# Kernel tuning notes

Measured on AMD Instinct MI355X. Metric: run time of the kernel, lower is better.

Reference implementation:

```python
import jax, jax.numpy as jnp
import numpy as np

EMB = 512
HEADS = 16
WH, WW = 8, 8
N = WH * WW
B = 2048
CPB_HID = 512
EPS = 1e-12


def _buffers():
    # continuous relative coords table, shape (1, 2*WH-1, 2*WW-1, 2)
    ch = np.arange(-(WH - 1), WH, dtype=np.float32)
    cw = np.arange(-(WW - 1), WW, dtype=np.float32)
    t = np.stack(np.meshgrid(ch, cw, indexing='ij')).transpose(1, 2, 0)[None].copy()
    t[..., 0] /= (WH - 1)
    t[..., 1] /= (WW - 1)
    t *= 8.0
    t = np.sign(t) * np.log2(np.abs(t) + 1.0) / np.log2(8.0)
    # relative position index, shape (N, N), values in [0, (2*WH-1)*(2*WW-1))
    coords = np.stack(np.meshgrid(np.arange(WH), np.arange(WW), indexing='ij'))
    cf = coords.reshape(2, -1)
    rel = (cf[:, :, None] - cf[:, None, :]).transpose(1, 2, 0).copy()
    rel[..., 0] += WH - 1
    rel[..., 1] += WW - 1
    rel[..., 0] *= 2 * WW - 1
    idx = rel.sum(-1)
    return jnp.asarray(t, jnp.float32), jnp.asarray(idx, jnp.int32)


def setup_inputs() -> dict:
    key = jax.random.key(0)
    ks = jax.random.split(key, 8)
    rel_table, rel_index = _buffers()
    s = 0.02
    return {
        'x': jax.random.normal(ks[0], (B, N, EMB), jnp.float32),
        'qkv_w': jax.random.normal(ks[1], (3 * EMB, EMB), jnp.float32) * s,
        'q_bias': jnp.zeros((EMB,), jnp.float32),
        'v_bias': jnp.zeros((EMB,), jnp.float32),
        'flex_attn': jnp.full((HEADS, 1, 1), np.log(10.0), jnp.float32),
        'cpb_w1': jax.random.normal(ks[2], (CPB_HID, 2), jnp.float32) * s,
        'cpb_b1': jnp.zeros((CPB_HID,), jnp.float32),
        'cpb_w2': jax.random.normal(ks[3], (HEADS, CPB_HID), jnp.float32) * s,
        'proj_w': jax.random.normal(ks[4], (EMB, EMB), jnp.float32) * s,
        'proj_b': jnp.zeros((EMB,), jnp.float32),
        'rel_table': rel_table,
        'rel_index': rel_index,
    }


def reference(x, qkv_w, q_bias, v_bias, flex_attn, cpb_w1, cpb_b1, cpb_w2,
              proj_w, proj_b, rel_table, rel_index):
    Bx, Nx, C = x.shape
    H = HEADS
    D = C // H
    # qkv with bias only on q and v (k bias is zero), as in the torch code
    qkv_bias = jnp.concatenate([q_bias, jnp.zeros_like(v_bias), v_bias])
    qkv = x @ qkv_w.T + qkv_bias                      # (B, N, 3C)
    qkv = qkv.reshape(Bx, Nx, 3, H, D).transpose(2, 0, 3, 1, 4)
    q, k, v = qkv[0], qkv[1], qkv[2]                  # each (B, H, N, D)
    # cosine attention: L2-normalize q and k
    qn = q / jnp.maximum(jnp.linalg.norm(q, axis=-1, keepdims=True), EPS)
    kn = k / jnp.maximum(jnp.linalg.norm(k, axis=-1, keepdims=True), EPS)
    attn = jnp.einsum('bhnd,bhmd->bhnm', qn, kn)      # (B, H, N, N)
    # learned per-head temperature, clamped at 1/0.01
    scale = jnp.exp(jnp.minimum(flex_attn, jnp.log(jnp.float32(100.0))))  # (H,1,1)
    attn = attn * scale[None]
    # continuous relative position bias via MLP + gather
    bias_tab = jax.nn.relu(rel_table @ cpb_w1.T + cpb_b1) @ cpb_w2.T      # (1, 2WH-1, 2WW-1, H)
    bias_tab = bias_tab.reshape(-1, H)
    bias = bias_tab[rel_index.reshape(-1)].reshape(Nx, Nx, H)
    bias = 16.0 * jax.nn.sigmoid(bias.transpose(2, 0, 1))                 # (H, N, N)
    attn = jax.nn.softmax(attn + bias[None], axis=-1)
    out = jnp.einsum('bhnm,bhmd->bhnd', attn, v)      # (B, H, N, D)
    out = out.transpose(0, 2, 1, 3).reshape(Bx, Nx, C)
    return out @ proj_w.T + proj_b
```

## Files before the change

### kernel.cpp

```cpp
#include <hip/hip_runtime.h>

using bf16x8 = __attribute__((ext_vector_type(8))) short;
using f32x4  = __attribute__((ext_vector_type(4))) float;
using f32x16 = __attribute__((ext_vector_type(16))) float;

static constexpr int EMB = 512, HEADS = 16, NTOK = 64, BWIN = 2048;
static constexpr int MROWS = BWIN * NTOK;
static constexpr int QKVN  = 3 * EMB;

__device__ __forceinline__ float bf2f(unsigned int u) {
  union { unsigned int i; float f; } c; c.i = u << 16; return c.f;
}
__device__ __forceinline__ unsigned short f2bf(float x) {
  union { float f; unsigned int i; } c; c.f = x;
  return (unsigned short)((c.i + 0x7fffu + ((c.i >> 16) & 1u)) >> 16);
}
__device__ __forceinline__ void gload_lds16(const void* g, void* l) {
  __builtin_amdgcn_global_load_lds((const __attribute__((address_space(1))) void*)g,
                                   (__attribute__((address_space(3))) void*)l, 16, 0, 0);
}
__device__ __forceinline__ unsigned int cvt_pk_bf16(float lo, float hi) {
  unsigned int d;
  asm("v_cvt_pk_bf16_f32 %0, %1, %2" : "=v"(d) : "v"(lo), "v"(hi));
  return d;
}

#define BARRIER() __builtin_amdgcn_s_barrier()
#define LGKM0()  do { asm volatile("s_waitcnt lgkmcnt(0)" ::: "memory"); \
                      __builtin_amdgcn_sched_barrier(0); } while (0)
#define VMCNT2() do { asm volatile("s_waitcnt vmcnt(2)" ::: "memory"); \
                      __builtin_amdgcn_sched_barrier(0); } while (0)

__global__ __launch_bounds__(256) void xcast(const float* __restrict__ x,
                                             unsigned short* __restrict__ xb) {
  size_t i = ((size_t)blockIdx.x * 256 + threadIdx.x) * 8;
  float4 a = *(const float4*)(x + i);
  float4 b = *(const float4*)(x + i + 4);
  ushort4 lo = make_ushort4(f2bf(a.x), f2bf(a.y), f2bf(a.z), f2bf(a.w));
  ushort4 hi = make_ushort4(f2bf(b.x), f2bf(b.y), f2bf(b.z), f2bf(b.w));
  *(ushort4*)(xb + i) = lo;
  *(ushort4*)(xb + i + 4) = hi;
}

__global__ void prep_weights(const float* __restrict__ qkv_w, const float* __restrict__ proj_w,
                             const float* __restrict__ q_bias, const float* __restrict__ v_bias,
                             unsigned short* __restrict__ wq, unsigned short* __restrict__ wp,
                             float* __restrict__ qkv_bias) {
  int i = blockIdx.x * 256 + threadIdx.x;
  wq[i] = f2bf(qkv_w[i]);
  if (i < EMB * EMB) wp[i] = f2bf(proj_w[i]);
  if (i < EMB) {
    qkv_bias[i]           = q_bias[i];
    qkv_bias[EMB + i]     = 0.f;
    qkv_bias[2 * EMB + i] = v_bias[i];
  }
}

__global__ __launch_bounds__(64) void cpb_mlp(const float* __restrict__ tbl,
                        const float* __restrict__ w1, const float* __restrict__ b1,
                        const float* __restrict__ w2, float* __restrict__ tab) {
  __shared__ float hid[512];
  const int p = blockIdx.x, t = threadIdx.x;
  const float t0 = tbl[p * 2], t1 = tbl[p * 2 + 1];
  #pragma unroll
  for (int s = 0; s < 8; ++s) {
    int j = t + s * 64;
    hid[j] = fmaxf(0.f, t0 * w1[j * 2] + t1 * w1[j * 2 + 1] + b1[j]);
  }
  __syncthreads();
  const int h = t >> 2, q = t & 3;
  float sum = 0.f;
  for (int j = q * 128; j < q * 128 + 128; ++j) sum += hid[j] * w2[h * 512 + j];
  sum += __shfl_xor(sum, 1);
  sum += __shfl_xor(sum, 2);
  if (q == 0) tab[p * 16 + h] = sum;
}

__global__ void cpb_expand(const float* __restrict__ tab, const int* __restrict__ rel_index,
                           float* __restrict__ biasT) {
  int e = blockIdx.x * 256 + threadIdx.x;
  int h = e >> 12, ij = e & 4095;
  int kk = ij >> 6, q = ij & 63;
  float x = tab[rel_index[q * 64 + kk] * 16 + h];
  biasT[e] = 16.f / (1.f + __expf(-x));
}

template<bool OUT_F32, int NBX, int KT>
__global__ __launch_bounds__(512, 2) void gemm256(const unsigned short* __restrict__ Ap,
    const unsigned short* __restrict__ Bp, const float* __restrict__ bias,
    void* __restrict__ Cp, int M, int N) {
  __shared__ unsigned short As[2][256 * 64];
  __shared__ unsigned short Bs[2][256 * 64];
  constexpr int NT = KT / 64;
  constexpr int NITER = NT / 2;
  const int t = threadIdx.x;
  const int l = t & 63, w = t >> 6;
  const int lr = l & 15, lg = l >> 4;
  const int q8 = gridDim.x >> 3;
  const int wgid = (blockIdx.x & 7) * q8 + (blockIdx.x >> 3);
  const int n0 = (wgid % NBX) * 256, m0 = (wgid / NBX) * 256;
  const int wm = (w >> 2) * 128, wn = (w & 3) * 64;
  const int ha128 = (w >> 2) * 128;
  const int srow = t >> 3;
  const int scol = ((t & 7) ^ (srow & 7)) << 3;
  const unsigned short* Abase = Ap + (size_t)m0 * KT;
  const unsigned short* Bbase = Bp + (size_t)n0 * KT;

  f32x4 acc[8][4];
  #pragma unroll
  for (int i = 0; i < 8; ++i)
    #pragma unroll
    for (int j = 0; j < 4; ++j) acc[i][j] = (f32x4){0.f, 0.f, 0.f, 0.f};
  bf16x8 afr[4][2], bfr[4][2];

  auto stage_half = [&](int d, int kt, int half, bool isA) {
    const unsigned short* g = (isA ? Abase : Bbase)
        + (size_t)(half * 128 + srow) * KT + kt * 64 + scol;
    unsigned short* lds = (isA ? &As[d][0] : &Bs[d][0]) + half * 8192 + (t >> 6) * 512;
    gload_lds16(g, lds);
    gload_lds16(g + (size_t)64 * KT, lds + 4096);
  };
  auto ldA4 = [&](int d, int mb) {
    #pragma unroll
    for (int m = 0; m < 4; ++m) {
      int row = ha128 + (mb + m) * 16 + lr;
      #pragma unroll
      for (int ks = 0; ks < 2; ++ks)
        afr[m][ks] = *(const bf16x8*)(&As[d][row * 64 + ((((ks << 2) + lg) ^ (lr & 7)) << 3)]);
    }
  };
  auto ldB2 = [&](int d, int nb) {
    #pragma unroll
    for (int n = 0; n < 2; ++n) {
      int row = wn + (nb + n) * 16 + lr;
      #pragma unroll
      for (int ks = 0; ks < 2; ++ks)
        bfr[nb + n][ks] = *(const bf16x8*)(&Bs[d][row * 64 + ((((ks << 2) + lg) ^ (lr & 7)) << 3)]);
    }
  };
  auto mfmaQ = [&](int mb, int nb) {
    __builtin_amdgcn_s_setprio(1);
    #pragma unroll
    for (int ks = 0; ks < 2; ++ks)
      #pragma unroll
      for (int m = 0; m < 4; ++m)
        #pragma unroll
        for (int n = 0; n < 2; ++n)
          acc[mb + m][nb + n] = __builtin_amdgcn_mfma_f32_16x16x32_bf16(
              afr[m][ks], bfr[nb + n][ks], acc[mb + m][nb + n], 0, 0, 0);
    __builtin_amdgcn_s_setprio(0);
  };

  stage_half(0, 0, 0, true);  stage_half(0, 0, 1, true);
  stage_half(0, 0, 0, false); stage_half(0, 0, 1, false);
  stage_half(1, (NT > 1 ? 1 : 0), 0, true);
  VMCNT2();
  BARRIER();

  for (int i = 0; i < NITER; ++i) {
    const int kt1 = 2 * i + 1;
    const int kt2 = (2 * i + 2 < NT) ? 2 * i + 2 : NT - 1;
    const int kt3 = (2 * i + 3 < NT) ? 2 * i + 3 : NT - 1;
    ldA4(0, 0); ldB2(0, 0);
    stage_half(1, kt1, 1, true);
    BARRIER(); LGKM0(); mfmaQ(0, 0); BARRIER();
    ldB2(0, 2);
    stage_half(1, kt1, 0, false);
    BARRIER(); LGKM0(); mfmaQ(0, 2); BARRIER();
    ldA4(0, 4);
    stage_half(1, kt1, 1, false);
    BARRIER(); LGKM0(); mfmaQ(4, 2); BARRIER();
    stage_half(0, kt2, 0, true);
    VMCNT2(); BARRIER(); mfmaQ(4, 0); BARRIER();
    ldA4(1, 0); ldB2(1, 0);
    stage_half(0, kt2, 1, true);
    BARRIER(); LGKM0(); mfmaQ(0, 0); BARRIER();
    ldB2(1, 2);
    stage_half(0, kt2, 0, false);
    BARRIER(); LGKM0(); mfmaQ(0, 2); BARRIER();
    ldA4(1, 4);
    stage_half(0, kt2, 1, false);
    BARRIER(); LGKM0(); mfmaQ(4, 2); BARRIER();
    stage_half(1, kt3, 0, true);
    VMCNT2(); BARRIER(); mfmaQ(4, 0); BARRIER();
  }

  #pragma unroll
  for (int mf = 0; mf < 8; ++mf)
    #pragma unroll
    for (int nf = 0; nf < 4; ++nf)
      #pragma unroll
      for (int r = 0; r < 4; ++r) {
        int mm = m0 + wm + mf * 16 + lg * 4 + r;
        int nn = n0 + wn + nf * 16 + lr;
        float v = acc[mf][nf][r] + bias[nn];
        if (OUT_F32) ((float*)Cp)[(size_t)mm * N + nn] = v;
        else ((unsigned short*)Cp)[(size_t)mm * N + nn] = f2bf(v);
      }
}

__global__ __launch_bounds__(64, 3) void attn_win(const unsigned short* __restrict__ qkv,
    const float* __restrict__ biasT, const float* __restrict__ flex,
    unsigned short* __restrict__ aout) {
  __shared__ __align__(16) unsigned short vT[32 * 64];
  const int l = threadIdx.x;
  const int lq = l & 31, hi = l >> 5;
  const int g = (blockIdx.x & 7) * (gridDim.x >> 3) + (blockIdx.x >> 3);
  const int b = g >> 4;
  const int h = g & 15;
  const unsigned short* base = qkv + (size_t)b * NTOK * QKVN;
  const float scale = __expf(fminf(flex[h], 4.6051701860f));

  {
    const uint4* vp = (const uint4*)(base + (size_t)l * QKVN + 2 * EMB + h * 32);
    uint4 v0 = vp[0], v1 = vp[1], v2 = vp[2], v3 = vp[3];
    unsigned int wd[16] = {v0.x, v0.y, v0.z, v0.w, v1.x, v1.y, v1.z, v1.w,
                           v2.x, v2.y, v2.z, v2.w, v3.x, v3.y, v3.z, v3.w};
    #pragma unroll
    for (int d = 0; d < 32; ++d) {
      unsigned short val = (d & 1) ? (unsigned short)(wd[d >> 1] >> 16)
                                   : (unsigned short)(wd[d >> 1] & 0xffffu);
      vT[d * 64 + (((l >> 3) ^ (d & 7)) << 3) + (l & 7)] = val;
    }
  }

  bf16x8 kfr[2][2], qfr[2][2];
  #pragma unroll
  for (int f = 0; f < 2; ++f) {
    #pragma unroll
    for (int which = 0; which < 2; ++which) {
      const unsigned short* rp = base + (size_t)(f * 32 + lq) * QKVN
                               + (which ? 0 : EMB) + h * 32 + hi * 8;
      uint4 r0 = *(const uint4*)rp;
      uint4 r1 = *(const uint4*)(rp + 16);
      unsigned int wd[8] = {r0.x, r0.y, r0.z, r0.w, r1.x, r1.y, r1.z, r1.w};
      float fv[16];
      #pragma unroll
      for (int e = 0; e < 8; ++e) {
        fv[2 * e]     = bf2f(wd[e] & 0xffffu);
        fv[2 * e + 1] = bf2f(wd[e] >> 16);
      }
      float ss = 0.f;
      #pragma unroll
      for (int e = 0; e < 16; ++e) ss += fv[e] * fv[e];
      ss += __shfl_xor(ss, 32);
      float inv = (which ? scale : 1.f) / fmaxf(sqrtf(ss), 1e-12f);
      bf16x8 f0, f1;
      #pragma unroll
      for (int e = 0; e < 8; ++e) {
        f0[e] = (short)f2bf(fv[e] * inv);
        f1[e] = (short)f2bf(fv[8 + e] * inv);
      }
      if (which) { qfr[f][0] = f0; qfr[f][1] = f1; }
      else       { kfr[f][0] = f0; kfr[f][1] = f1; }
    }
  }

  asm volatile("" ::: "memory");

  bf16x8 bv[4];
  #pragma unroll
  for (int c = 0; c < 4; ++c)
    bv[c] = *(const bf16x8*)(&vT[lq * 64 + ((((2 * c + hi) ^ (lq & 7))) << 3)]);

  const f32x16 z16 = (f32x16)(0.f);

  #pragma unroll
  for (int qf = 0; qf < 2; ++qf) {
    f32x16 s0 = __builtin_amdgcn_mfma_f32_32x32x16_bf16(kfr[0][0], qfr[qf][0], z16, 0, 0, 0);
    s0 = __builtin_amdgcn_mfma_f32_32x32x16_bf16(kfr[0][1], qfr[qf][1], s0, 0, 0, 0);
    f32x16 s1 = __builtin_amdgcn_mfma_f32_32x32x16_bf16(kfr[1][0], qfr[qf][0], z16, 0, 0, 0);
    s1 = __builtin_amdgcn_mfma_f32_32x32x16_bf16(kfr[1][1], qfr[qf][1], s1, 0, 0, 0);

    float p[32];
    const float* bt = biasT + (size_t)h * 4096 + qf * 32 + lq;
    #pragma unroll
    for (int r = 0; r < 16; ++r) {
      int kkb = (r & 3) + 8 * (r >> 2) + 4 * hi;
      p[r]      = s0[r] + bt[kkb * 64];
      p[16 + r] = s1[r] + bt[(32 + kkb) * 64];
    }
    float mx = p[0];
    #pragma unroll
    for (int e = 1; e < 32; ++e) mx = fmaxf(mx, p[e]);
    mx = fmaxf(mx, __shfl_xor(mx, 32));
    float sum = 0.f;
    #pragma unroll
    for (int e = 0; e < 32; ++e) { p[e] = __expf(p[e] - mx); sum += p[e]; }
    sum += __shfl_xor(sum, 32);
    const float inv = 1.f / sum;
    #pragma unroll
    for (int e = 0; e < 32; ++e) p[e] *= inv;

    unsigned int wp_[2][8], sw[2][8];
    #pragma unroll
    for (int kf = 0; kf < 2; ++kf)
      #pragma unroll
      for (int m = 0; m < 8; ++m) {
        wp_[kf][m] = cvt_pk_bf16(p[kf * 16 + 2 * m], p[kf * 16 + 2 * m + 1]);
        sw[kf][m]  = (unsigned int)__builtin_amdgcn_ds_bpermute(
                        ((l ^ 32) & 63) << 2, (int)wp_[kf][m]);
      }
    f32x16 oacc = z16;
    #pragma unroll
    for (int c = 0; c < 4; ++c) {
      const int kf = c >> 1, mlo = (c & 1) * 4;
      unsigned int d0 = hi ? sw[kf][mlo + 2] : wp_[kf][mlo + 0];
      unsigned int d1 = hi ? sw[kf][mlo + 3] : wp_[kf][mlo + 1];
      unsigned int d2 = hi ? wp_[kf][mlo + 2] : sw[kf][mlo + 0];
      unsigned int d3 = hi ? wp_[kf][mlo + 3] : sw[kf][mlo + 1];
      union { uint4 u; bf16x8 v; } pa;
      pa.u = make_uint4(d0, d1, d2, d3);
      oacc = __builtin_amdgcn_mfma_f32_32x32x16_bf16(pa.v, bv[c], oacc, 0, 0, 0);
    }
    #pragma unroll
    for (int r = 0; r < 16; ++r) {
      int q = qf * 32 + (r & 3) + 8 * (r >> 2) + 4 * hi;
      aout[(size_t)(b * NTOK + q) * EMB + h * 32 + lq] = f2bf(oacc[r]);
    }
  }
}

extern "C" void kernel_launch(void* const* d_in, const int* in_sizes, int n_in,
                              void* d_out, int out_size, void* d_ws, size_t ws_size,
                              hipStream_t stream) {
  const float* x         = (const float*)d_in[0];
  const float* qkv_w     = (const float*)d_in[1];
  const float* q_bias    = (const float*)d_in[2];
  const float* v_bias    = (const float*)d_in[3];
  const float* flex      = (const float*)d_in[4];
  const float* cpb_w1    = (const float*)d_in[5];
  const float* cpb_b1    = (const float*)d_in[6];
  const float* cpb_w2    = (const float*)d_in[7];
  const float* proj_w    = (const float*)d_in[8];
  const float* proj_b    = (const float*)d_in[9];
  const float* rel_table = (const float*)d_in[10];
  const int*   rel_index = (const int*)d_in[11];

  char* ws = (char*)d_ws;
  unsigned short* qkv_bf = (unsigned short*)(ws + 0);
  unsigned short* xb     = (unsigned short*)(ws + 402653184ull);
  unsigned short* ao_bf  = (unsigned short*)(ws + 402653184ull);
  unsigned short* wq_bf  = (unsigned short*)(ws + 536870912ull);
  unsigned short* wp_bf  = (unsigned short*)(ws + 538443776ull);
  float* qkv_bias        = (float*)(ws + 538968064ull);
  float* tab             = (float*)(ws + 538974208ull);
  float* biasT           = (float*)(ws + 538988608ull);

  xcast<<<32768, 256, 0, stream>>>(x, xb);
  prep_weights<<<3072, 256, 0, stream>>>(qkv_w, proj_w, q_bias, v_bias, wq_bf, wp_bf, qkv_bias);
  cpb_mlp<<<225, 64, 0, stream>>>(rel_table, cpb_w1, cpb_b1, cpb_w2, tab);
  cpb_expand<<<256, 256, 0, stream>>>(tab, rel_index, biasT);
  gemm256<false, 6, EMB><<<3072, 512, 0, stream>>>(
      xb, wq_bf, qkv_bias, (void*)qkv_bf, MROWS, QKVN);
  attn_win<<<BWIN * HEADS, 64, 0, stream>>>(qkv_bf, biasT, flex, ao_bf);
  gemm256<true, 2, EMB><<<1024, 512, 0, stream>>>(
      ao_bf, wp_bf, proj_b, d_out, MROWS, EMB);
}
```

Before: 637.3 us.

## Fuse fp32-to-bf16 cast of x into the QKV GEMM A-tile load

```diff
diff --git a/kernel.cpp b/kernel.cpp
--- a/kernel.cpp
+++ b/kernel.cpp
@@ -26,21 +26,15 @@
 }
 
 #define BARRIER() __builtin_amdgcn_s_barrier()
+#define SCHED0()  __builtin_amdgcn_sched_barrier(0)
 #define LGKM0()  do { asm volatile("s_waitcnt lgkmcnt(0)" ::: "memory"); \
                       __builtin_amdgcn_sched_barrier(0); } while (0)
 #define VMCNT2() do { asm volatile("s_waitcnt vmcnt(2)" ::: "memory"); \
                       __builtin_amdgcn_sched_barrier(0); } while (0)
-
-__global__ __launch_bounds__(256) void xcast(const float* __restrict__ x,
-                                             unsigned short* __restrict__ xb) {
-  size_t i = ((size_t)blockIdx.x * 256 + threadIdx.x) * 8;
-  float4 a = *(const float4*)(x + i);
-  float4 b = *(const float4*)(x + i + 4);
-  ushort4 lo = make_ushort4(f2bf(a.x), f2bf(a.y), f2bf(a.z), f2bf(a.w));
-  ushort4 hi = make_ushort4(f2bf(b.x), f2bf(b.y), f2bf(b.z), f2bf(b.w));
-  *(ushort4*)(xb + i) = lo;
-  *(ushort4*)(xb + i + 4) = hi;
-}
+#define VMCNT4() do { asm volatile("s_waitcnt vmcnt(4)" ::: "memory"); \
+                      __builtin_amdgcn_sched_barrier(0); } while (0)
+#define VMCNT8() do { asm volatile("s_waitcnt vmcnt(8)" ::: "memory"); \
+                      __builtin_amdgcn_sched_barrier(0); } while (0)
 
 __global__ void prep_weights(const float* __restrict__ qkv_w, const float* __restrict__ proj_w,
                              const float* __restrict__ q_bias, const float* __restrict__ v_bias,
@@ -83,6 +77,146 @@
   int kk = ij >> 6, q = ij & 63;
   float x = tab[rel_index[q * 64 + kk] * 16 + h];
   biasT[e] = 16.f / (1.f + __expf(-x));
+}
+
+template<int NBX, int KT>
+__global__ __launch_bounds__(512, 2) void gemm256_af32(const float* __restrict__ Af,
+    const unsigned short* __restrict__ Bp, const float* __restrict__ bias,
+    unsigned short* __restrict__ Cp, int M, int N) {
+  __shared__ unsigned short As[2][256 * 64];
+  __shared__ unsigned short Bs[2][256 * 64];
+  constexpr int NT = KT / 64;
+  constexpr int NITER = NT / 2;
+  const int t = threadIdx.x;
+  const int l = t & 63, w = t >> 6;
+  const int lr = l & 15, lg = l >> 4;
+  const int q8 = gridDim.x >> 3;
+  const int wgid = (blockIdx.x & 7) * q8 + (blockIdx.x >> 3);
+  const int n0 = (wgid % NBX) * 256, m0 = (wgid / NBX) * 256;
+  const int wm = (w >> 2) * 128, wn = (w & 3) * 64;
+  const int ha128 = (w >> 2) * 128;
+  const int srow = t >> 3;
+  const int scol = ((t & 7) ^ (srow & 7)) << 3;
+  const int arow = t >> 2, aq = t & 3;
+  const float* Ab = Af + (size_t)m0 * KT;
+  const unsigned short* Bbase = Bp + (size_t)n0 * KT;
+
+  f32x4 acc[8][4];
+  #pragma unroll
+  for (int i = 0; i < 8; ++i)
+    #pragma unroll
+    for (int j = 0; j < 4; ++j) acc[i][j] = (f32x4){0.f, 0.f, 0.f, 0.f};
+  bf16x8 afr[4][2], bfr[4][2];
+  float4 rC0[4], rC1[4], rN0[4], rN1[4], rD0[4], rD1[4];
+
+  auto BS = [&](int d, int kt, int half) {
+    const unsigned short* g = Bbase + (size_t)(half * 128 + srow) * KT + kt * 64 + scol;
+    unsigned short* lds = &Bs[d][0] + half * 8192 + w * 512;
+    gload_lds16(g, lds);
+    gload_lds16(g + (size_t)64 * KT, lds + 4096);
+  };
+  auto AL = [&](int kt, int half, float4* R) {
+    const float* g = Ab + (size_t)(half * 128 + arow) * KT + kt * 64 + aq * 16;
+    R[0] = ((const float4*)g)[0]; R[1] = ((const float4*)g)[1];
+    R[2] = ((const float4*)g)[2]; R[3] = ((const float4*)g)[3];
+  };
+  auto AW = [&](int d, int half, const float4* R) {
+    unsigned short* dst = &As[d][(half * 128 + arow) * 64];
+    const float* f = (const float*)R;
+    unsigned int dw[8];
+    #pragma unroll
+    for (int m2 = 0; m2 < 8; ++m2) dw[m2] = cvt_pk_bf16(f[2 * m2], f[2 * m2 + 1]);
+    union { uint4 u; bf16x8 v; } lo, hi;
+    lo.u = make_uint4(dw[0], dw[1], dw[2], dw[3]);
+    hi.u = make_uint4(dw[4], dw[5], dw[6], dw[7]);
+    const int r7 = arow & 7;
+    *(bf16x8*)(dst + ((aq * 2) ^ r7) * 8)     = lo.v;
+    *(bf16x8*)(dst + ((aq * 2 + 1) ^ r7) * 8) = hi.v;
+  };
+  auto ldA4 = [&](int d, int mb) {
+    #pragma unroll
+    for (int m = 0; m < 4; ++m) {
+      int row = ha128 + (mb + m) * 16 + lr;
+      #pragma unroll
+      for (int ks = 0; ks < 2; ++ks)
+        afr[m][ks] = *(const bf16x8*)(&As[d][row * 64 + ((((ks << 2) + lg) ^ (lr & 7)) << 3)]);
+    }
+  };
+  auto ldB2 = [&](int d, int nb) {
+    #pragma unroll
+    for (int n = 0; n < 2; ++n) {
+      int row = wn + (nb + n) * 16 + lr;
+      #pragma unroll
+      for (int ks = 0; ks < 2; ++ks)
+        bfr[nb + n][ks] = *(const bf16x8*)(&Bs[d][row * 64 + ((((ks << 2) + lg) ^ (lr & 7)) << 3)]);
+    }
+  };
+  auto mfmaQ = [&](int mb, int nb) {
+    __builtin_amdgcn_s_setprio(1);
+    #pragma unroll
+    for (int ks = 0; ks < 2; ++ks)
+      #pragma unroll
+      for (int m = 0; m < 4; ++m)
+        #pragma unroll
+        for (int n = 0; n < 2; ++n)
+          acc[mb + m][nb + n] = __builtin_amdgcn_mfma_f32_16x16x32_bf16(
+              afr[m][ks], bfr[nb + n][ks], acc[mb + m][nb + n], 0, 0, 0);
+    __builtin_amdgcn_s_setprio(0);
+  };
+
+  AL(0, 0, rN0); AL(0, 1, rN1); SCHED0();
+  BS(0, 0, 0); BS(0, 0, 1); SCHED0();
+  AW(0, 0, rN0); AW(0, 1, rN1); SCHED0();
+  AL((NT > 1 ? 1 : 0), 0, rC0); AL((NT > 1 ? 1 : 0), 1, rC1); SCHED0();
+  VMCNT8();
+  LGKM0();
+  BARRIER();
+
+  #pragma unroll
+  for (int i = 0; i < NITER; ++i) {
+    const int ktb = 2 * i + 1;
+    const int ktc = (2 * i + 2 < NT) ? 2 * i + 2 : NT - 1;
+    const int ktd = (2 * i + 3 < NT) ? 2 * i + 3 : NT - 1;
+    ldA4(0, 0); ldB2(0, 0);
+    AW(1, 0, rC0); SCHED0();
+    BARRIER(); LGKM0(); mfmaQ(0, 0); BARRIER();
+    ldB2(0, 2);
+    BS(1, ktb, 0); SCHED0();
+    AW(1, 1, rC1); SCHED0();
+    AL(ktc, 0, rN0); SCHED0();
+    BARRIER(); LGKM0(); mfmaQ(0, 2); BARRIER();
+    ldA4(0, 4);
+    BS(1, ktb, 1); SCHED0();
+    AL(ktc, 1, rN1); SCHED0();
+    BARRIER(); LGKM0(); mfmaQ(4, 2); BARRIER();
+    VMCNT4(); BARRIER(); mfmaQ(4, 0); BARRIER();
+    ldA4(1, 0); ldB2(1, 0);
+    AW(0, 0, rN0); SCHED0();
+    BARRIER(); LGKM0(); mfmaQ(0, 0); BARRIER();
+    ldB2(1, 2);
+    BS(0, ktc, 0); SCHED0();
+    AW(0, 1, rN1); SCHED0();
+    AL(ktd, 0, rD0); SCHED0();
+    BARRIER(); LGKM0(); mfmaQ(0, 2); BARRIER();
+    ldA4(1, 4);
+    BS(0, ktc, 1); SCHED0();
+    AL(ktd, 1, rD1); SCHED0();
+    BARRIER(); LGKM0(); mfmaQ(4, 2); BARRIER();
+    VMCNT4(); BARRIER(); mfmaQ(4, 0); BARRIER();
+    #pragma unroll
+    for (int j = 0; j < 4; ++j) { rC0[j] = rD0[j]; rC1[j] = rD1[j]; }
+  }
+
+  #pragma unroll
+  for (int mf = 0; mf < 8; ++mf)
+    #pragma unroll
+    for (int nf = 0; nf < 4; ++nf)
+      #pragma unroll
+      for (int r = 0; r < 4; ++r) {
+        int mm = m0 + wm + mf * 16 + lg * 4 + r;
+        int nn = n0 + wn + nf * 16 + lr;
+        Cp[(size_t)mm * N + nn] = f2bf(acc[mf][nf][r] + bias[nn]);
+      }
 }
 
 template<bool OUT_F32, int NBX, int KT>
@@ -339,7 +473,6 @@
 
   char* ws = (char*)d_ws;
   unsigned short* qkv_bf = (unsigned short*)(ws + 0);
-  unsigned short* xb     = (unsigned short*)(ws + 402653184ull);
   unsigned short* ao_bf  = (unsigned short*)(ws + 402653184ull);
   unsigned short* wq_bf  = (unsigned short*)(ws + 536870912ull);
   unsigned short* wp_bf  = (unsigned short*)(ws + 538443776ull);
@@ -347,12 +480,11 @@
   float* tab             = (float*)(ws + 538974208ull);
   float* biasT           = (float*)(ws + 538988608ull);
 
-  xcast<<<32768, 256, 0, stream>>>(x, xb);
   prep_weights<<<3072, 256, 0, stream>>>(qkv_w, proj_w, q_bias, v_bias, wq_bf, wp_bf, qkv_bias);
   cpb_mlp<<<225, 64, 0, stream>>>(rel_table, cpb_w1, cpb_b1, cpb_w2, tab);
   cpb_expand<<<256, 256, 0, stream>>>(tab, rel_index, biasT);
-  gemm256<false, 6, EMB><<<3072, 512, 0, stream>>>(
-      xb, wq_bf, qkv_bias, (void*)qkv_bf, MROWS, QKVN);
+  gemm256_af32<6, EMB><<<3072, 512, 0, stream>>>(
+      x, wq_bf, qkv_bias, qkv_bf, MROWS, QKVN);
   attn_win<<<BWIN * HEADS, 64, 0, stream>>>(qkv_bf, biasT, flex, ao_bf);
   gemm256<true, 2, EMB><<<1024, 512, 0, stream>>>(
       ao_bf, wp_bf, proj_b, d_out, MROWS, EMB);
```

Measured after the change: 634.8 us. About the same (-0.4%).

## Process four heads per attention block with LDS-staged Q/K loads

Applied to the files above, without the earlier changes.

```diff
diff --git a/kernel.cpp b/kernel.cpp
--- a/kernel.cpp
+++ b/kernel.cpp
@@ -199,21 +199,35 @@
       }
 }
 
-__global__ __launch_bounds__(64, 3) void attn_win(const unsigned short* __restrict__ qkv,
+__global__ __launch_bounds__(256, 3) void attn_win4(const unsigned short* __restrict__ qkv,
     const float* __restrict__ biasT, const float* __restrict__ flex,
     unsigned short* __restrict__ aout) {
-  __shared__ __align__(16) unsigned short vT[32 * 64];
-  const int l = threadIdx.x;
+  __shared__ __align__(16) unsigned short kq[16384];
+  __shared__ __align__(16) unsigned short vTall[4][2048];
+  const int t = threadIdx.x;
+  const int l = t & 63, w = t >> 6;
   const int lq = l & 31, hi = l >> 5;
   const int g = (blockIdx.x & 7) * (gridDim.x >> 3) + (blockIdx.x >> 3);
-  const int b = g >> 4;
-  const int h = g & 15;
+  const int b = g >> 2;
+  const int p = g & 3;
+  const int h = p * 4 + w;
   const unsigned short* base = qkv + (size_t)b * NTOK * QKVN;
   const float scale = __expf(fminf(flex[h], 4.6051701860f));
 
+  const uint4* vp = (const uint4*)(base + (size_t)l * QKVN + 2 * EMB + h * 32);
+  uint4 v0 = vp[0], v1 = vp[1], v2 = vp[2], v3 = vp[3];
+
+  #pragma unroll
+  for (int i = 0; i < 8; ++i) {
+    int sl  = (w * 8 + i) * 64 + l;
+    int tok = sl >> 5, sec = (sl >> 4) & 1, phys = sl & 15;
+    int log = phys ^ (tok & 15);
+    gload_lds16(base + (size_t)tok * QKVN + (sec ? EMB : 0) + p * 128 + log * 8,
+                kq + (size_t)(w * 8 + i) * 512);
+  }
+
+  unsigned short* vT = vTall[w];
   {
-    const uint4* vp = (const uint4*)(base + (size_t)l * QKVN + 2 * EMB + h * 32);
-    uint4 v0 = vp[0], v1 = vp[1], v2 = vp[2], v3 = vp[3];
     unsigned int wd[16] = {v0.x, v0.y, v0.z, v0.w, v1.x, v1.y, v1.z, v1.w,
                            v2.x, v2.y, v2.z, v2.w, v3.x, v3.y, v3.z, v3.w};
     #pragma unroll
@@ -223,16 +237,20 @@
       vT[d * 64 + (((l >> 3) ^ (d & 7)) << 3) + (l & 7)] = val;
     }
   }
+  __syncthreads();
 
   bf16x8 kfr[2][2], qfr[2][2];
   #pragma unroll
   for (int f = 0; f < 2; ++f) {
     #pragma unroll
     for (int which = 0; which < 2; ++which) {
-      const unsigned short* rp = base + (size_t)(f * 32 + lq) * QKVN
-                               + (which ? 0 : EMB) + h * 32 + hi * 8;
-      uint4 r0 = *(const uint4*)rp;
-      uint4 r1 = *(const uint4*)(rp + 16);
+      const int tok = f * 32 + lq;
+      const int sec = which ? 0 : 1;
+      const unsigned short* row = kq + tok * 256 + sec * 128;
+      const int ls0 = w * 4 + hi;
+      const int ls1 = w * 4 + 2 + hi;
+      uint4 r0 = *(const uint4*)(row + ((ls0 ^ (tok & 15)) << 3));
+      uint4 r1 = *(const uint4*)(row + ((ls1 ^ (tok & 15)) << 3));
       unsigned int wd[8] = {r0.x, r0.y, r0.z, r0.w, r1.x, r1.y, r1.z, r1.w};
       float fv[16];
       #pragma unroll
@@ -256,8 +274,6 @@
     }
   }
 
-  asm volatile("" ::: "memory");
-
   bf16x8 bv[4];
   #pragma unroll
   for (int c = 0; c < 4; ++c)
@@ -272,32 +288,32 @@
     f32x16 s1 = __builtin_amdgcn_mfma_f32_32x32x16_bf16(kfr[1][0], qfr[qf][0], z16, 0, 0, 0);
     s1 = __builtin_amdgcn_mfma_f32_32x32x16_bf16(kfr[1][1], qfr[qf][1], s1, 0, 0, 0);
 
-    float p[32];
+    float p2[32];
     const float* bt = biasT + (size_t)h * 4096 + qf * 32 + lq;
     #pragma unroll
     for (int r = 0; r < 16; ++r) {
       int kkb = (r & 3) + 8 * (r >> 2) + 4 * hi;
-      p[r]      = s0[r] + bt[kkb * 64];
-      p[16 + r] = s1[r] + bt[(32 + kkb) * 64];
-    }
-    float mx = p[0];
-    #pragma unroll
-    for (int e = 1; e < 32; ++e) mx = fmaxf(mx, p[e]);
+      p2[r]      = s0[r] + bt[kkb * 64];
+      p2[16 + r] = s1[r] + bt[(32 + kkb) * 64];
+    }
+    float mx = p2[0];
+    #pragma unroll
+    for (int e = 1; e < 32; ++e) mx = fmaxf(mx, p2[e]);
     mx = fmaxf(mx, __shfl_xor(mx, 32));
     float sum = 0.f;
     #pragma unroll
-    for (int e = 0; e < 32; ++e) { p[e] = __expf(p[e] - mx); sum += p[e]; }
+    for (int e = 0; e < 32; ++e) { p2[e] = __expf(p2[e] - mx); sum += p2[e]; }
     sum += __shfl_xor(sum, 32);
     const float inv = 1.f / sum;
     #pragma unroll
-    for (int e = 0; e < 32; ++e) p[e] *= inv;
+    for (int e = 0; e < 32; ++e) p2[e] *= inv;
 
     unsigned int wp_[2][8], sw[2][8];
     #pragma unroll
     for (int kf = 0; kf < 2; ++kf)
       #pragma unroll
       for (int m = 0; m < 8; ++m) {
-        wp_[kf][m] = cvt_pk_bf16(p[kf * 16 + 2 * m], p[kf * 16 + 2 * m + 1]);
+        wp_[kf][m] = cvt_pk_bf16(p2[kf * 16 + 2 * m], p2[kf * 16 + 2 * m + 1]);
         sw[kf][m]  = (unsigned int)__builtin_amdgcn_ds_bpermute(
                         ((l ^ 32) & 63) << 2, (int)wp_[kf][m]);
       }
@@ -353,7 +369,7 @@
   cpb_expand<<<256, 256, 0, stream>>>(tab, rel_index, biasT);
   gemm256<false, 6, EMB><<<3072, 512, 0, stream>>>(
       xb, wq_bf, qkv_bias, (void*)qkv_bf, MROWS, QKVN);
-  attn_win<<<BWIN * HEADS, 64, 0, stream>>>(qkv_bf, biasT, flex, ao_bf);
+  attn_win4<<<BWIN * 4, 256, 0, stream>>>(qkv_bf, biasT, flex, ao_bf);
   gemm256<true, 2, EMB><<<1024, 512, 0, stream>>>(
       ao_bf, wp_bf, proj_b, d_out, MROWS, EMB);
 }
```

Measured after the change: 632.2 us, median of 2. No clear change (-0.8%).
